# Performance work log

Hardware: AMD Instinct MI355X
Metric: run time of the kernel (lower is better)

The kernel has to match this reference:

```python
import jax, jax.numpy as jnp
import numpy as np

N_NODES = 100000
IN_CH = 128
HID_CH = 128
N_EDGES = 1600000


def setup_inputs() -> dict:
    key = jax.random.key(0)
    ks = jax.random.split(key, 8)
    x = jax.random.normal(ks[0], (N_NODES, IN_CH), dtype=jnp.float32)
    edge_index = jax.random.randint(ks[1], (2, N_EDGES), 0, N_NODES, dtype=jnp.int64)
    s1 = 1.0 / np.sqrt(IN_CH)
    s2 = 1.0 / np.sqrt(HID_CH)
    # SAGEConv layer 1: lin_l (aggregated neighbors, has bias), lin_r (root)
    Wl1 = jax.random.uniform(ks[2], (IN_CH, HID_CH), jnp.float32, -s1, s1)
    Wr1 = jax.random.uniform(ks[3], (IN_CH, HID_CH), jnp.float32, -s1, s1)
    b1 = jnp.zeros((HID_CH,), jnp.float32)
    # SAGEConv layer 2
    Wl2 = jax.random.uniform(ks[4], (HID_CH, HID_CH), jnp.float32, -s2, s2)
    Wr2 = jax.random.uniform(ks[5], (HID_CH, HID_CH), jnp.float32, -s2, s2)
    b2 = jnp.zeros((HID_CH,), jnp.float32)
    return {"x": x, "edge_index": edge_index,
            "Wl1": Wl1, "Wr1": Wr1, "b1": b1,
            "Wl2": Wl2, "Wr2": Wr2, "b2": b2}


def _sage_conv(x, src, dst, inv_deg, Wl, Wr, b):
    # mean aggregation of source-node features into destination nodes
    agg = jax.ops.segment_sum(x[src], dst, num_segments=N_NODES)  # [N, d]
    mean = agg * inv_deg[:, None]
    # out = lin_l(mean_neighbors) + lin_r(x)
    return mean @ Wl + x @ Wr + b


def reference(x, edge_index, Wl1, Wr1, b1, Wl2, Wr2, b2):
    src = edge_index[0]
    dst = edge_index[1]
    deg = jax.ops.segment_sum(jnp.ones_like(dst, dtype=jnp.float32), dst,
                              num_segments=N_NODES)
    inv_deg = 1.0 / jnp.maximum(deg, 1.0)
    h = jax.nn.relu(_sage_conv(x, src, dst, inv_deg, Wl1, Wr1, b1))
    # F.dropout(p=0.2, training=False) is identity in eval mode
    h = jax.nn.relu(_sage_conv(h, src, dst, inv_deg, Wl2, Wr2, b2))
    return h
```

## Files before the change

### kernel.cpp

```cpp
#include <hip/hip_runtime.h>

#define NN 100000
#define NE 1600000
#define CH 128

#define PART 512
#define NP 196
#define PCAP 8704
#define EPB 4096
#define NB 391
#define SCAP 64
#define SLAB 3072

typedef __attribute__((ext_vector_type(8))) short bf16x8;
typedef __attribute__((ext_vector_type(4))) float f32x4;
typedef unsigned int uint;
typedef unsigned short ushort;

__device__ __forceinline__ ushort f2b(float f) {
    uint u = __builtin_bit_cast(uint, f);
    uint r = (u + 0x7fff + ((u >> 16) & 1)) >> 16;
    return (ushort)r;
}
__device__ __forceinline__ float blo(uint v) { return __builtin_bit_cast(float, v << 16); }
__device__ __forceinline__ float bhi(uint v) { return __builtin_bit_cast(float, v & 0xffff0000u); }

__device__ __forceinline__ void acc8(float* a, uint4 v) {
    a[0] += blo(v.x); a[1] += bhi(v.x);
    a[2] += blo(v.y); a[3] += bhi(v.y);
    a[4] += blo(v.z); a[5] += bhi(v.z);
    a[6] += blo(v.w); a[7] += bhi(v.w);
}


__global__ __launch_bounds__(1024) void k_bin(const int4* __restrict__ src4, const int4* __restrict__ dst4,
                                              uint* __restrict__ pcnt, uint* __restrict__ pairbuf) {
    __shared__ uint slots[NP * SCAP];
    __shared__ uint lcnt[NP];
    __shared__ uint lbase[NP];
    int tid = threadIdx.x;
    if (tid < NP) lcnt[tid] = 0;
    __syncthreads();
    int e4 = blockIdx.x * 1024 + tid;
    if (e4 < NE / 4) {
        int4 d4 = dst4[e4];
        int4 s4 = src4[e4];
        int dd[4] = {d4.x, d4.y, d4.z, d4.w};
        int ss[4] = {s4.x, s4.y, s4.z, s4.w};
        #pragma unroll
        for (int j = 0; j < 4; ++j) {
            int p = dd[j] >> 9;
            uint pair = ((uint)(dd[j] & 511) << 17) | (uint)ss[j];
            uint pos = atomicAdd(&lcnt[p], 1u);
            if (pos < SCAP) slots[p * SCAP + pos] = pair;
        }
    }
    __syncthreads();
    if (tid < NP) {
        uint c = lcnt[tid];
        c = c < SCAP ? c : SCAP;
        lcnt[tid] = c;
        lbase[tid] = atomicAdd(&pcnt[tid], c);
    }
    __syncthreads();
    for (int t = tid; t < NP * SCAP; t += 1024) {
        int p = t >> 6;
        uint s = (uint)(t & (SCAP - 1));
        if (s < lcnt[p]) {
            uint idx = lbase[p] + s;
            if (idx < PCAP) pairbuf[(size_t)p * PCAP + idx] = slots[t];
        }
    }
}


__global__ __launch_bounds__(512) void k_csr(const uint* __restrict__ pcnt, const uint* __restrict__ pairbuf,
                                             int* __restrict__ nbrG, uint* __restrict__ pack,
                                             uint* __restrict__ ord) {
    __shared__ uint pairs[PCAP];
    __shared__ uint cnt[PART];
    __shared__ uint rankv[PART];
    __shared__ uint srow[PART + 1];
    __shared__ uint tsum[PART];
    __shared__ uint hbase[64];
    int tid = threadIdx.x;
    int p = blockIdx.x;
    uint tot = pcnt[p];
    tot = tot < PCAP ? tot : PCAP;
    for (uint i = tid; i < tot; i += 512) pairs[i] = pairbuf[(size_t)p * PCAP + i];
    cnt[tid] = 0;
    if (tid < 64) hbase[tid] = 0;
    __syncthreads();
    for (uint i = tid; i < tot; i += 512) atomicAdd(&cnt[pairs[i] >> 17], 1u);
    __syncthreads();
    uint deg = cnt[tid];
    uint db = deg < 63 ? deg : 63;
    atomicAdd(&hbase[db], 1u);
    __syncthreads();
    if (tid == 0) {
        uint s = 0;
        for (int i = 0; i < 64; ++i) { uint h = hbase[i]; hbase[i] = s; s += h; }
    }
    __syncthreads();
    uint rk = atomicAdd(&hbase[db], 1u);
    rankv[tid] = rk;
    tsum[rk] = deg;
    __syncthreads();
    uint sd = tsum[tid];
    for (int off = 1; off < 512; off <<= 1) {
        uint t = (tid >= off) ? tsum[tid - off] : 0;
        __syncthreads();
        tsum[tid] += t;
        __syncthreads();
    }
    srow[tid] = tsum[tid] - sd;
    if (tid == 511) srow[512] = tsum[511];
    __syncthreads();
    cnt[tid] = 0;
    __syncthreads();
    for (uint i = tid; i < tot; i += 512) {
        uint u = pairs[i];
        uint dl = u >> 17;
        uint pos = srow[rankv[dl]] + atomicAdd(&cnt[dl], 1u);
        nbrG[(size_t)p * PCAP + pos] = (int)(u & 0x1FFFFu);
    }
    {
        int n = p * PART + tid;
        uint q = rankv[tid];
        pack[(size_t)p * PART + q] = ((uint)(p * PCAP) + srow[q]) | (deg << 21);
        ord[(size_t)p * PART + q] = (n < NN) ? (uint)n : (uint)NN;
    }
}


__global__ __launch_bounds__(256) void k_castx(const float* __restrict__ x, ushort* __restrict__ xb) {
    int n = blockIdx.x * 256 + threadIdx.x;
    int p = blockIdx.y;
    if (n >= NN) return;
    const float4* sp = (const float4*)(x + (size_t)n * 128 + p * 32);
    uint4 o[4];
    ushort* op = (ushort*)o;
    #pragma unroll
    for (int q = 0; q < 8; ++q) {
        float4 v = sp[q];
        op[q * 4 + 0] = f2b(v.x);
        op[q * 4 + 1] = f2b(v.y);
        op[q * 4 + 2] = f2b(v.z);
        op[q * 4 + 3] = f2b(v.w);
    }
    uint4* dp = (uint4*)(xb + ((size_t)p * NN + n) * 32);
    #pragma unroll
    for (int q = 0; q < 4; ++q) dp[q] = o[q];
}

__global__ __launch_bounds__(256) void k_castw(const float* __restrict__ Wl1, const float* __restrict__ Wr1,
                                               const float* __restrict__ Wl2, const float* __restrict__ Wr2,
                                               ushort* __restrict__ BtK1, ushort* __restrict__ BtK2) {
    int i = blockIdx.x * 256 + threadIdx.x;
    const float* Wl = blockIdx.y ? Wl2 : Wl1;
    const float* Wr = blockIdx.y ? Wr2 : Wr1;
    ushort* BtK = blockIdx.y ? BtK2 : BtK1;
    int c = i & 31;
    int n = (i >> 5) & 127;
    int kt = i >> 12;
    int k = kt * 32 + c;
    float v = (k < 128) ? Wl[k * 128 + n] : Wr[(k - 128) * 128 + n];
    BtK[i] = f2b(v);
}


__global__ __launch_bounds__(256) void k_agg(const uint4* __restrict__ feat, const int* __restrict__ nbrG,
                                             const uint* __restrict__ pack, const uint* __restrict__ ord,
                                             uint4* __restrict__ outb) {
    __shared__ int sl[SLAB];
    __shared__ int sh_s0, sh_cnt;
    int plane = blockIdx.x;
    int nb = blockIdx.y * 64;
    int tid = threadIdx.x;
    int n = nb + (tid >> 2);
    int h = tid & 3;
    if (tid == 0) {
        uint u0 = pack[nb];
        uint u1 = pack[nb + 63];
        int s0 = (int)(u0 & 0x1FFFFFu);
        sh_s0 = s0;
        sh_cnt = (int)(u1 & 0x1FFFFFu) + (int)(u1 >> 21) - s0;
    }
    __syncthreads();
    int s0 = sh_s0, scnt = sh_cnt;
    bool staged = scnt <= SLAB;
    if (staged) {
        for (int i = tid; i < scnt; i += 256) sl[i] = nbrG[s0 + i];
    }
    __syncthreads();
    uint u = pack[n];
    int s = (int)(u & 0x1FFFFFu);
    int d = (int)(u >> 21);
    const char* fb = (const char*)feat + ((size_t)plane * NN) * 64;
    uint hoff = (uint)h * 16;
    float a[8] = {};
    if (staged) {
        const int* bp = sl + (s - s0);
        int i = 0;
        for (; i + 8 <= d; i += 8) {
            uint off[8];
            uint4 v[8];
            #pragma unroll
            for (int j = 0; j < 8; ++j) off[j] = ((uint)bp[i + j] << 6) | hoff;
            #pragma unroll
            for (int j = 0; j < 8; ++j) v[j] = *(const uint4*)(fb + off[j]);
            #pragma unroll
            for (int j = 0; j < 8; ++j) acc8(a, v[j]);
        }
        for (; i < d; ++i) acc8(a, *(const uint4*)(fb + (((uint)bp[i] << 6) | hoff)));
    } else {
        const int* bp = nbrG + s;
        int i = 0;
        for (; i + 4 <= d; i += 4) {
            uint o0 = ((uint)bp[i] << 6) | hoff;
            uint o1 = ((uint)bp[i + 1] << 6) | hoff;
            uint o2 = ((uint)bp[i + 2] << 6) | hoff;
            uint o3 = ((uint)bp[i + 3] << 6) | hoff;
            uint4 v0 = *(const uint4*)(fb + o0);
            uint4 v1 = *(const uint4*)(fb + o1);
            uint4 v2 = *(const uint4*)(fb + o2);
            uint4 v3 = *(const uint4*)(fb + o3);
            acc8(a, v0);
            acc8(a, v1);
            acc8(a, v2);
            acc8(a, v3);
        }
        for (; i < d; ++i) acc8(a, *(const uint4*)(fb + (((uint)bp[i] << 6) | hoff)));
    }
    int on = (int)ord[n];
    if (on >= NN) return;
    float id = 1.0f / fmaxf((float)d, 1.0f);
    uint4 r;
    r.x = (uint)f2b(a[0] * id) | ((uint)f2b(a[1] * id) << 16);
    r.y = (uint)f2b(a[2] * id) | ((uint)f2b(a[3] * id) << 16);
    r.z = (uint)f2b(a[4] * id) | ((uint)f2b(a[5] * id) << 16);
    r.w = (uint)f2b(a[6] * id) | ((uint)f2b(a[7] * id) << 16);
    outb[((size_t)plane * NN + on) * 4 + h] = r;
}


template <bool WB16>
__global__ __launch_bounds__(256) void k_gemm(const ushort* __restrict__ Am, const ushort* Ax,
                                              const ushort* __restrict__ BtK, const float* __restrict__ bias,
                                              void* outp, int M) {
    int lane = threadIdx.x & 63;
    int wave = threadIdx.x >> 6;
    int bm = blockIdx.x * 128 + wave * 32;
    int l16 = lane & 15;
    int lk8 = (lane >> 4) * 8;

    f32x4 acc[2][8] = {};
    #pragma unroll
    for (int kt = 0; kt < 8; ++kt) {
        const ushort* A = (kt < 4) ? Am : Ax;
        int p = kt & 3;
        bf16x8 af[2];
        #pragma unroll
        for (int mt = 0; mt < 2; ++mt) {
            int row = bm + mt * 16 + l16;
            row = row < M ? row : M - 1;
            af[mt] = *(const bf16x8*)(A + ((size_t)p * NN + row) * 32 + lk8);
        }
        const ushort* Bk = BtK + (size_t)kt * 128 * 32;
        #pragma unroll
        for (int nt = 0; nt < 8; ++nt) {
            bf16x8 bfr = *(const bf16x8*)(Bk + (size_t)(nt * 16 + l16) * 32 + lk8);
            acc[0][nt] = __builtin_amdgcn_mfma_f32_16x16x32_bf16(af[0], bfr, acc[0][nt], 0, 0, 0);
            acc[1][nt] = __builtin_amdgcn_mfma_f32_16x16x32_bf16(af[1], bfr, acc[1][nt], 0, 0, 0);
        }
    }
    int mr0 = (lane >> 4) * 4;
    #pragma unroll
    for (int mt = 0; mt < 2; ++mt) {
        #pragma unroll
        for (int r = 0; r < 4; ++r) {
            int m = bm + mt * 16 + mr0 + r;
            if (m < M) {
                #pragma unroll
                for (int nt = 0; nt < 8; ++nt) {
                    float v = acc[mt][nt][r] + bias[nt * 16 + l16];
                    v = v > 0.f ? v : 0.f;
                    if (WB16) {
                        int ch = nt * 16 + l16;
                        ((ushort*)outp)[((size_t)(ch >> 5) * NN + m) * 32 + (ch & 31)] = f2b(v);
                    } else {
                        ((float*)outp)[(size_t)m * 128 + nt * 16 + l16] = v;
                    }
                }
            }
        }
    }
}


static inline size_t alignup(size_t x) { return (x + 255) & ~(size_t)255; }

extern "C" void kernel_launch(void* const* d_in, const int* in_sizes, int n_in,
                              void* d_out, int out_size, void* d_ws, size_t ws_size,
                              hipStream_t stream) {
    const float* x   = (const float*)d_in[0];
    const int* edge  = (const int*)d_in[1];
    const float* Wl1 = (const float*)d_in[2];
    const float* Wr1 = (const float*)d_in[3];
    const float* b1  = (const float*)d_in[4];
    const float* Wl2 = (const float*)d_in[5];
    const float* Wr2 = (const float*)d_in[6];
    const float* b2  = (const float*)d_in[7];
    float* out = (float*)d_out;

    const int* srcp = edge;
    const int* dstp = edge + NE;

    uint* pairbuf = (uint*)d_out;
    int* nbrG = (int*)d_out + (size_t)NP * PCAP;

    char* w = (char*)d_ws;
    uint* pcnt = (uint*)w;     w += alignup((size_t)NP * 4);
    uint* pack = (uint*)w;     w += alignup((size_t)NP * PART * 4);
    uint* ordm = (uint*)w;     w += alignup((size_t)NP * PART * 4);
    ushort* xb = (ushort*)w;   w += alignup((size_t)NN * CH * 2);
    ushort* mb = (ushort*)w;   w += alignup((size_t)NN * CH * 2);
    ushort* BtK1 = (ushort*)w; w += alignup((size_t)128 * 256 * 2);
    ushort* BtK2 = (ushort*)w; w += alignup((size_t)128 * 256 * 2);

    hipMemsetAsync(pcnt, 0, (size_t)NP * 4, stream);

    k_bin<<<NB, 1024, 0, stream>>>((const int4*)srcp, (const int4*)dstp, pcnt, pairbuf);
    k_csr<<<NP, 512, 0, stream>>>(pcnt, pairbuf, nbrG, pack, ordm);

    k_castx<<<dim3((NN + 255) / 256, 4), 256, 0, stream>>>(x, xb);
    k_castw<<<dim3(128, 2), 256, 0, stream>>>(Wl1, Wr1, Wl2, Wr2, BtK1, BtK2);

    int gg = (NN + 127) / 128;
    dim3 ag(4, NP * 8);
    k_agg<<<ag, 256, 0, stream>>>((const uint4*)xb, nbrG, pack, ordm, (uint4*)mb);
    k_gemm<true><<<gg, 256, 0, stream>>>(mb, xb, BtK1, b1, (void*)xb, NN);
    k_agg<<<ag, 256, 0, stream>>>((const uint4*)xb, nbrG, pack, ordm, (uint4*)mb);
    k_gemm<false><<<gg, 256, 0, stream>>>(mb, xb, BtK2, b2, (void*)out, NN);
}
```

Baseline: 358.7 us.

## Interleave degree-sorted node slots across waves and stage neighbor lists per wave

The partition kernel now places nodes in a strided slot order so that each wave of 16 nodes gets a round-robin mix of degree-ranked chunks. Each block now spreads its degree mix evenly across its four waves instead of giving one wave all the heavy nodes. The aggregation kernel stages neighbor indices in a per-wave shared slab of 1024 entries instead of one block-wide slab, computing bounds per wave without a leader thread. This aims to reduce load imbalance between waves and avoid the block-wide staging fallback. It relies on the variable rk being defined in the hidden code, and on the per-wave slab being large enough.

```diff
diff --git a/kernel.cpp b/kernel.cpp
--- a/kernel.cpp
+++ b/kernel.cpp
@@ -10,7 +10,7 @@
 #define EPB 4096
 #define NB 391
 #define SCAP 64
-#define SLAB 3072
+#define WSLAB 1024
 
 typedef __attribute__((ext_vector_type(8))) short bf16x8;
 typedef __attribute__((ext_vector_type(4))) float f32x4;
@@ -126,9 +126,10 @@
     }
     {
         int n = p * PART + tid;
-        uint q = rankv[tid];
-        pack[(size_t)p * PART + q] = ((uint)(p * PCAP) + srow[q]) | (deg << 21);
-        ord[(size_t)p * PART + q] = (n < NN) ? (uint)n : (uint)NN;
+        uint c = rk >> 4, jj = rk & 15;
+        uint slot = (c & 7) * 64 + (c >> 3) * 16 + jj;
+        pack[(size_t)p * PART + slot] = ((uint)(p * PCAP) + srow[rk]) | (deg << 21);
+        ord[(size_t)p * PART + slot] = (n < NN) ? (uint)n : (uint)NN;
     }
 }
 
@@ -172,45 +173,44 @@
 __global__ __launch_bounds__(256) void k_agg(const uint4* __restrict__ feat, const int* __restrict__ nbrG,
                                              const uint* __restrict__ pack, const uint* __restrict__ ord,
                                              uint4* __restrict__ outb) {
-    __shared__ int sl[SLAB];
-    __shared__ int sh_s0, sh_cnt;
+    __shared__ int sl[4 * WSLAB];
     int plane = blockIdx.x;
     int nb = blockIdx.y * 64;
     int tid = threadIdx.x;
-    int n = nb + (tid >> 2);
-    int h = tid & 3;
-    if (tid == 0) {
-        uint u0 = pack[nb];
-        uint u1 = pack[nb + 63];
-        int s0 = (int)(u0 & 0x1FFFFFu);
-        sh_s0 = s0;
-        sh_cnt = (int)(u1 & 0x1FFFFFu) + (int)(u1 >> 21) - s0;
-    }
-    __syncthreads();
-    int s0 = sh_s0, scnt = sh_cnt;
-    bool staged = scnt <= SLAB;
+    int wv = tid >> 6;
+    int lane = tid & 63;
+    int j = lane >> 2;
+    int h = lane & 3;
+    int wbase = nb + wv * 16;
+    uint u0 = pack[wbase];
+    uint u15 = pack[wbase + 15];
+    int s0 = (int)(u0 & 0x1FFFFFu);
+    int send = (int)(u15 & 0x1FFFFFu) + (int)(u15 >> 21);
+    int scnt = send - s0;
+    bool staged = scnt <= WSLAB;
+    int* slw = sl + wv * WSLAB;
     if (staged) {
-        for (int i = tid; i < scnt; i += 256) sl[i] = nbrG[s0 + i];
-    }
-    __syncthreads();
-    uint u = pack[n];
+        for (int i = lane; i < scnt; i += 64) slw[i] = nbrG[s0 + i];
+    }
+    __syncthreads();
+    uint u = pack[wbase + j];
     int s = (int)(u & 0x1FFFFFu);
     int d = (int)(u >> 21);
     const char* fb = (const char*)feat + ((size_t)plane * NN) * 64;
     uint hoff = (uint)h * 16;
     float a[8] = {};
     if (staged) {
-        const int* bp = sl + (s - s0);
+        const int* bp = slw + (s - s0);
         int i = 0;
         for (; i + 8 <= d; i += 8) {
             uint off[8];
             uint4 v[8];
             #pragma unroll
-            for (int j = 0; j < 8; ++j) off[j] = ((uint)bp[i + j] << 6) | hoff;
+            for (int jj = 0; jj < 8; ++jj) off[jj] = ((uint)bp[i + jj] << 6) | hoff;
             #pragma unroll
-            for (int j = 0; j < 8; ++j) v[j] = *(const uint4*)(fb + off[j]);
+            for (int jj = 0; jj < 8; ++jj) v[jj] = *(const uint4*)(fb + off[jj]);
             #pragma unroll
-            for (int j = 0; j < 8; ++j) acc8(a, v[j]);
+            for (int jj = 0; jj < 8; ++jj) acc8(a, v[jj]);
         }
         for (; i < d; ++i) acc8(a, *(const uint4*)(fb + (((uint)bp[i] << 6) | hoff)));
     } else {
@@ -232,7 +232,7 @@
         }
         for (; i < d; ++i) acc8(a, *(const uint4*)(fb + (((uint)bp[i] << 6) | hoff)));
     }
-    int on = (int)ord[n];
+    int on = (int)ord[wbase + j];
     if (on >= NN) return;
     float id = 1.0f / fmaxf((float)d, 1.0f);
     uint4 r;
```

Result: faster. 349.7 us (-2.5%).
